# Optimization experiments

Hardware: AMD Instinct MI355X
Metric: run time of the kernel (lower is better)

Reference implementation:

```python
import jax, jax.numpy as jnp
import numpy as np

T, B, I, H = 512, 64, 1024, 1024
G = 4 * H + 1  # 4 LSTM gates + 1 boundary gate (HM-LSTM)
STDV = 1.0 / np.sqrt(H)


def setup_inputs() -> dict:
    key = jax.random.key(0)
    ks = jax.random.split(key, 5)
    u = lambda k, shape: jax.random.uniform(k, shape, jnp.float32, -STDV, STDV)
    return {
        "x": jax.random.normal(ks[0], (T, B, I), jnp.float32),
        "W_ih": u(ks[1], (G, I)),
        "W_hh": u(ks[2], (G, H)),
        "b_ih": u(ks[3], (G,)),
        "b_hh": u(ks[4], (G,)),
    }


def reference(x, W_ih, W_hh, b_ih, b_hh):
    h_dim = W_hh.shape[1]
    # Precompute input contribution for all timesteps in one big GEMM: [T,B,G]
    gx_all = jnp.einsum("tbi,gi->tbg", x, W_ih) + b_ih + b_hh
    Bsz = x.shape[1]
    h0 = jnp.zeros((Bsz, h_dim), x.dtype)
    c0 = jnp.zeros((Bsz, h_dim), x.dtype)

    def step(carry, gx):
        h, c = carry
        g = gx + h @ W_hh.T  # [B, 4H+1]
        i = jax.nn.sigmoid(g[:, :h_dim])
        f = jax.nn.sigmoid(g[:, h_dim:2 * h_dim])
        gg = jnp.tanh(g[:, 2 * h_dim:3 * h_dim])
        o = jax.nn.sigmoid(g[:, 3 * h_dim:4 * h_dim])
        z = jax.nn.sigmoid(g[:, 4 * h_dim:])  # [B,1] boundary gate
        ig = i * gg
        # HM-LSTM soft boundary: FLUSH (c=i*g) when z->1, UPDATE otherwise
        c_new = z * ig + (1.0 - z) * (f * c + ig)
        h_new = o * jnp.tanh(c_new)
        return (h_new, c_new), h_new

    (hT, cT), out = jax.lax.scan(step, (h0, c0), gx_all)
    return out, hT, cT
```

## Files before the change

### kernel.cpp

```cpp
#include <hip/hip_runtime.h>
#include <cstdint>
#include <cstddef>

typedef unsigned short u16;
typedef short bf16x8 __attribute__((ext_vector_type(8)));
typedef u16   u16x8  __attribute__((ext_vector_type(8)));
typedef float f32x4  __attribute__((ext_vector_type(4)));

#define NT  512
#define NB  64
#define NH  1024
#define NTB 32768
#define G4  4096

#define AS1C(p) ((const __attribute__((address_space(1))) void*)(p))
#define AS3(p)  ((__attribute__((address_space(3))) void*)(p))

__device__ __forceinline__ float b2f(u16 u){
  return __uint_as_float(((unsigned)u) << 16);
}
__device__ __forceinline__ u16 f2b(float f){
  unsigned u = __float_as_uint(f);
  return (u16)((u + 0x7fffu + ((u >> 16) & 1u)) >> 16);
}
__device__ __forceinline__ float fsigmoid(float x){
  return __builtin_amdgcn_rcpf(1.f + __builtin_amdgcn_exp2f(-1.442695041f * x));
}
__device__ __forceinline__ float ftanh(float x){
  return 2.f * __builtin_amdgcn_rcpf(1.f + __builtin_amdgcn_exp2f(-2.885390082f * x)) - 1.f;
}

__global__ void cvt_bf16(const float* __restrict__ in, u16* __restrict__ out, int n8){
  int stride = gridDim.x * blockDim.x;
  for (int i = blockIdx.x * blockDim.x + threadIdx.x; i < n8; i += stride){
    const float4* p = (const float4*)(in + (size_t)i * 8);
    float4 a = p[0], b = p[1];
    u16x8 r;
    r[0]=f2b(a.x); r[1]=f2b(a.y); r[2]=f2b(a.z); r[3]=f2b(a.w);
    r[4]=f2b(b.x); r[5]=f2b(b.y); r[6]=f2b(b.z); r[7]=f2b(b.w);
    *(u16x8*)(out + (size_t)i * 8) = r;
  }
}

__global__ void zpre_kernel(const float* __restrict__ x, const float* __restrict__ Wih,
                            const float* __restrict__ b_ih, const float* __restrict__ b_hh,
                            float* __restrict__ zp){
  int gw   = (blockIdx.x * 256 + threadIdx.x) >> 6;
  int lane = threadIdx.x & 63;
  const float* wz = Wih + (size_t)4096 * 1024;
  float4 wv[4];
  #pragma unroll
  for (int j = 0; j < 4; ++j) wv[j] = *(const float4*)&wz[lane*16 + j*4];
  float bz = b_ih[4096] + b_hh[4096];
  for (int r = gw; r < NTB; r += 1024){
    const float* xr = x + (size_t)r * 1024 + lane * 16;
    float s = 0.f;
    #pragma unroll
    for (int j = 0; j < 4; ++j){
      float4 xv = *(const float4*)&xr[j*4];
      s += xv.x*wv[j].x + xv.y*wv[j].y + xv.z*wv[j].z + xv.w*wv[j].w;
    }
    #pragma unroll
    for (int o = 32; o > 0; o >>= 1) s += __shfl_down(s, o);
    if (lane == 0) zp[r] = s + bz;
  }
}

template<typename GT>
__global__ __launch_bounds__(256, 2) void gemm_gx(
    const u16* __restrict__ Xb, const u16* __restrict__ Wb,
    const float* __restrict__ b_ih, const float* __restrict__ b_hh,
    GT* __restrict__ gx)
{
  __shared__ u16 As[128*32];
  __shared__ u16 Bs[128*32];
  const int tid  = threadIdx.x;
  const int lane = tid & 63, wave = tid >> 6;
  const int wr = wave >> 1, wc = wave & 1;
  const int m0 = (blockIdx.x & 255) * 128;
  const int n0 = (blockIdx.x >> 8) * 128;
  const int srow = wave * 16 + (lane >> 2);
  const int scol = (lane & 3) * 8;
  const u16* gA = Xb + (size_t)(m0 + srow) * 1024 + scol;
  const u16* gB = Wb + (size_t)(n0 + srow) * 1024 + scol;
  char* lA = (char*)As + wave * 1024;
  char* lB = (char*)Bs + wave * 1024;
  const int fr = lane & 15, fo = (lane >> 4) * 8;

  f32x4 acc[4][4] = {};
  for (int k0 = 0; k0 < 1024; k0 += 32){
    __syncthreads();
    __builtin_amdgcn_global_load_lds(AS1C(gA + k0),            AS3(lA),        16, 0, 0);
    __builtin_amdgcn_global_load_lds(AS1C(gA + 64*1024 + k0),  AS3(lA + 4096), 16, 0, 0);
    __builtin_amdgcn_global_load_lds(AS1C(gB + k0),            AS3(lB),        16, 0, 0);
    __builtin_amdgcn_global_load_lds(AS1C(gB + 64*1024 + k0),  AS3(lB + 4096), 16, 0, 0);
    __syncthreads();
    bf16x8 a[4], b[4];
    #pragma unroll
    for (int mi = 0; mi < 4; ++mi)
      a[mi] = *(const bf16x8*)&As[(wr*64 + mi*16 + fr)*32 + fo];
    #pragma unroll
    for (int ni = 0; ni < 4; ++ni)
      b[ni] = *(const bf16x8*)&Bs[(wc*64 + ni*16 + fr)*32 + fo];
    #pragma unroll
    for (int mi = 0; mi < 4; ++mi)
      #pragma unroll
      for (int ni = 0; ni < 4; ++ni)
        acc[mi][ni] = __builtin_amdgcn_mfma_f32_16x16x32_bf16(a[mi], b[ni], acc[mi][ni], 0, 0, 0);
  }
  const int orow = (lane >> 4) * 4, ocol = lane & 15;
  #pragma unroll
  for (int ni = 0; ni < 4; ++ni){
    const int g = n0 + wc*64 + ni*16 + ocol;
    const float bias = b_ih[g] + b_hh[g];
    #pragma unroll
    for (int mi = 0; mi < 4; ++mi){
      const size_t rb = (size_t)(m0 + wr*64 + mi*16 + orow);
      #pragma unroll
      for (int r = 0; r < 4; ++r){
        float v = acc[mi][ni][r] + bias;
        if constexpr (sizeof(GT) == 4)
          __builtin_nontemporal_store(v, (float*)gx + (rb + r)*G4 + g);
        else
          __builtin_nontemporal_store(f2b(v), (u16*)gx + (rb + r)*G4 + g);
      }
    }
  }
}

__device__ __forceinline__ float ld_gx(const float* p){ return __builtin_nontemporal_load(p); }
__device__ __forceinline__ float ld_gx(const u16* p){ return b2f(__builtin_nontemporal_load(p)); }

template<typename GT>
__global__ __launch_bounds__(256, 1) void hmlstm_scan(
    const u16* __restrict__ Whh, const GT* __restrict__ gx,
    const float* __restrict__ zpre, u16* __restrict__ hbase,
    float* __restrict__ out, unsigned* __restrict__ bar)
{
  const int tid  = threadIdx.x;
  const int lane = tid & 63, wave = tid >> 6;
  const int wg = blockIdx.x;
  const int mb = wg >> 6, hb = wg & 63;
  const int fr = lane & 15, hi4 = lane >> 4;
  const int b_l = tid >> 4, h_l = tid & 15;
  const int browg = mb*16 + b_l;

  __shared__ u16  hs[16*1024];
  __shared__ float glds[4][16][16];
  __shared__ float zpart[4][16];
  __shared__ u16  wz[1024];

  ((unsigned long long*)wz)[tid] = ((const unsigned long long*)(Whh + (size_t)4096*1024))[tid];

  const int grow = wave*1024 + hb*16 + fr;
  bf16x8 Bw[32];
  #pragma unroll
  for (int kc = 0; kc < 32; ++kc)
    Bw[kc] = *(const bf16x8*)&Whh[(size_t)grow*1024 + kc*32 + hi4*8];
  #pragma unroll
  for (int kc = 0; kc < 32; ++kc)
    asm volatile("" : "+v"(Bw[kc]));

  {
    u16* p = hbase + (size_t)mb*16384 + hb*256 + tid;
    unsigned z = 0;
    asm volatile("global_store_short %0, %1, off sc0 sc1" :: "v"(p), "v"(z) : "memory");
    asm volatile("s_waitcnt vmcnt(0)" ::: "memory");
  }
  unsigned* myflag = bar + mb*256 + hb*4 + wave;
  const unsigned* gflags = bar + mb*256;
  if (lane == 0){
    unsigned one = 1;
    asm volatile("global_store_dword %0, %1, off sc0 sc1" :: "v"(myflag), "v"(one) : "memory");
  }

  float c_reg = 0.f;

  for (int t = 0; t < NT; ++t){
    const u16* hc = hbase + (size_t)t * 65536;
    u16*       hn = hbase + (size_t)(t + 1) * 65536;

    float gxl[4];
    const GT* gp = gx + ((size_t)t*64 + mb*16 + hi4*4)*G4 + wave*1024 + hb*16 + fr;
    #pragma unroll
    for (int r = 0; r < 4; ++r) gxl[r] = ld_gx(gp + (size_t)r*G4);
    float zpc = zpre[t*64 + browg];

    {
      const unsigned* fp = gflags + lane*4;
      unsigned tgt = (unsigned)(t + 1);
      uint4 fv;
      unsigned mn;
      do {
        asm volatile("global_load_dwordx4 %0, %1, off sc0 sc1\n\ts_waitcnt vmcnt(0)"
                     : "=v"(fv) : "v"(fp) : "memory");
        mn = min(min(fv.x, fv.y), min(fv.z, fv.w));
      } while (!__all((int)(mn >= tgt)));
      __builtin_amdgcn_sched_barrier(0);
    }

    {
      const char* gsrc = (const char*)hc + (size_t)mb * 32768;
      char* hsB = (char*)hs;
      #pragma unroll
      for (int j = 0; j < 8; ++j){
        int chunk = wave*8 + j;
        int row   = chunk >> 1;
        int srcoff = row*2048 + ((((chunk & 1)*64 + lane)*16) ^ ((row & 7) << 4));
        __builtin_amdgcn_global_load_lds(AS1C(gsrc + srcoff), AS3(hsB + chunk*1024), 16, 0, 0);
      }
    }
    asm volatile("s_waitcnt vmcnt(0)" ::: "memory");
    __builtin_amdgcn_sched_barrier(0);
    __syncthreads();

    f32x4 acc[4] = {}, az = {};
    #pragma unroll
    for (int kc = 0; kc < 32; ++kc){
      bf16x8 a = *(const bf16x8*)((char*)hs + fr*2048 + ((kc*64 + hi4*16) ^ ((fr&7)<<4)));
      acc[kc & 3] = __builtin_amdgcn_mfma_f32_16x16x32_bf16(a, Bw[kc], acc[kc & 3], 0, 0, 0);
    }
    #pragma unroll
    for (int q = 0; q < 8; ++q){
      int kcz = wave*8 + q;
      bf16x8 a  = *(const bf16x8*)((char*)hs + fr*2048 + ((kcz*64 + hi4*16) ^ ((fr&7)<<4)));
      bf16x8 bz = *(const bf16x8*)&wz[kcz*32 + hi4*8];
      az = __builtin_amdgcn_mfma_f32_16x16x32_bf16(a, bz, az, 0, 0, 0);
    }
    f32x4 ac = (acc[0] + acc[1]) + (acc[2] + acc[3]);

    #pragma unroll
    for (int r = 0; r < 4; ++r){
      float v = ac[r] + gxl[r];
      float s = (wave == 2) ? ftanh(v) : fsigmoid(v);
      glds[wave][hi4*4 + r][fr] = s;
    }
    if (fr == 0){
      #pragma unroll
      for (int r = 0; r < 4; ++r) zpart[wave][hi4*4 + r] = az[r];
    }
    __syncthreads();

    float iv = glds[0][b_l][h_l], fvg = glds[1][b_l][h_l];
    float gv = glds[2][b_l][h_l], ov = glds[3][b_l][h_l];
    float zs = zpart[0][b_l] + zpart[1][b_l] + zpart[2][b_l] + zpart[3][b_l];
    float zv = fsigmoid(zpc + zs);
    float ig = iv * gv;
    float cn = zv*ig + (1.f - zv)*(fvg*c_reg + ig);
    float hv_ = ov * ftanh(cn);
    c_reg = cn;
    const int hoff = browg*1024 + hb*16 + h_l;

    {
      unsigned hv16 = (unsigned)f2b(hv_);
      asm volatile("global_store_short %0, %1, off sc0 sc1" :: "v"(hn + hoff), "v"(hv16) : "memory");
      asm volatile("s_waitcnt vmcnt(0)" ::: "memory");
      if (lane == 0){
        unsigned pv = (unsigned)(t + 2);
        asm volatile("global_store_dword %0, %1, off sc0 sc1" :: "v"(myflag), "v"(pv) : "memory");
      }
    }

    __builtin_nontemporal_store(hv_, out + (size_t)t*65536 + hoff);
    if (t == NT-1){
      out[(size_t)NT*65536 + hoff] = hv_;
      out[(size_t)NT*65536 + 65536 + hoff] = cn;
    }
  }
}

extern "C" void kernel_launch(void* const* d_in, const int* in_sizes, int n_in,
                              void* d_out, int out_size, void* d_ws, size_t ws_size,
                              hipStream_t stream)
{
  (void)in_sizes; (void)n_in; (void)out_size;
  const float* x    = (const float*)d_in[0];
  const float* Wih  = (const float*)d_in[1];
  const float* Whh  = (const float*)d_in[2];
  const float* b_ih = (const float*)d_in[3];
  const float* b_hh = (const float*)d_in[4];
  float* out = (float*)d_out;

  size_t off = 0;
  auto alloc = [&](size_t bytes)->void*{
    void* p = (char*)d_ws + off;
    off = (off + bytes + 255) & ~(size_t)255;
    return p;
  };
  u16*  xb    = (u16*) alloc((size_t)NTB*1024*2);
  u16*  wihb  = (u16*) alloc((size_t)4097*1024*2);
  u16*  whhb  = (u16*) alloc((size_t)4097*1024*2);
  u16*  hbase = (u16*) alloc((size_t)(NT+1)*65536*2);
  float* zp   = (float*)alloc((size_t)NTB*4);
  unsigned* bar = (unsigned*)alloc(4096);
  bool g32 = (ws_size >= off + (size_t)NTB*G4*4);
  void* gxp = (char*)d_ws + off;

  hipMemsetAsync(bar, 0, 4096, stream);
  cvt_bf16<<<dim3(2048), dim3(256), 0, stream>>>(x,   xb,   NTB*1024/8);
  cvt_bf16<<<dim3(512),  dim3(256), 0, stream>>>(Wih, wihb, 4097*1024/8);
  cvt_bf16<<<dim3(512),  dim3(256), 0, stream>>>(Whh, whhb, 4097*1024/8);
  zpre_kernel<<<dim3(256), dim3(256), 0, stream>>>(x, Wih, b_ih, b_hh, zp);
  if (g32){
    gemm_gx<float><<<dim3(8192), dim3(256), 0, stream>>>(xb, wihb, b_ih, b_hh, (float*)gxp);
    hmlstm_scan<float><<<dim3(256), dim3(256), 0, stream>>>(whhb, (const float*)gxp, zp,
                                                            hbase, out, bar);
  } else {
    gemm_gx<u16><<<dim3(8192), dim3(256), 0, stream>>>(xb, wihb, b_ih, b_hh, (u16*)gxp);
    hmlstm_scan<u16><<<dim3(256), dim3(256), 0, stream>>>(whhb, (const u16*)gxp, zp,
                                                          hbase, out, bar);
  }
}
```

Before: 3.902 ms.

## Pack timestep tag with bf16 hidden state to replace flag barrier

Each hidden value is now stored as a 32-bit word holding the bf16 value and a 16-bit timestep tag. Consumers poll the data itself and re-read only the rows whose tags are stale, so the separate flag array, the store-wait-flag sequence and the flag spin loop are gone. The per-step hidden history becomes a double buffer, and the gx/zpre loads are issued as async asm loads so they overlap the polling. This doubles the bytes read per step for h and moves the LDS fill from a direct global-to-LDS copy to register unpacking, and it relies on the 16-bit tag staying unambiguous and on 64-bit ordering within the double buffer.

```diff
diff --git a/kernel.cpp b/kernel.cpp
--- a/kernel.cpp
+++ b/kernel.cpp
@@ -128,14 +128,11 @@
   }
 }
 
-__device__ __forceinline__ float ld_gx(const float* p){ return __builtin_nontemporal_load(p); }
-__device__ __forceinline__ float ld_gx(const u16* p){ return b2f(__builtin_nontemporal_load(p)); }
-
 template<typename GT>
 __global__ __launch_bounds__(256, 1) void hmlstm_scan(
     const u16* __restrict__ Whh, const GT* __restrict__ gx,
-    const float* __restrict__ zpre, u16* __restrict__ hbase,
-    float* __restrict__ out, unsigned* __restrict__ bar)
+    const float* __restrict__ zpre, unsigned* __restrict__ hdw,
+    float* __restrict__ out)
 {
   const int tid  = threadIdx.x;
   const int lane = tid & 63, wave = tid >> 6;
@@ -162,56 +159,76 @@
     asm volatile("" : "+v"(Bw[kc]));
 
   {
-    u16* p = hbase + (size_t)mb*16384 + hb*256 + tid;
-    unsigned z = 0;
-    asm volatile("global_store_short %0, %1, off sc0 sc1" :: "v"(p), "v"(z) : "memory");
-    asm volatile("s_waitcnt vmcnt(0)" ::: "memory");
-  }
-  unsigned* myflag = bar + mb*256 + hb*4 + wave;
-  const unsigned* gflags = bar + mb*256;
-  if (lane == 0){
-    unsigned one = 1;
-    asm volatile("global_store_dword %0, %1, off sc0 sc1" :: "v"(myflag), "v"(one) : "memory");
+    unsigned* p = hdw + (size_t)browg*1024 + hb*16 + h_l;
+    unsigned v0 = 1u;
+    asm volatile("global_store_dword %0, %1, off sc0 sc1" :: "v"(p), "v"(v0) : "memory");
   }
 
   float c_reg = 0.f;
 
   for (int t = 0; t < NT; ++t){
-    const u16* hc = hbase + (size_t)t * 65536;
-    u16*       hn = hbase + (size_t)(t + 1) * 65536;
-
-    float gxl[4];
-    const GT* gp = gx + ((size_t)t*64 + mb*16 + hi4*4)*G4 + wave*1024 + hb*16 + fr;
-    #pragma unroll
-    for (int r = 0; r < 4; ++r) gxl[r] = ld_gx(gp + (size_t)r*G4);
-    float zpc = zpre[t*64 + browg];
-
+    const unsigned* src = hdw + (size_t)(t & 1) * 65536;
+    unsigned*       dst = hdw + (size_t)((t + 1) & 1) * 65536;
+    const unsigned tgt = (unsigned)(t + 1);
+
+    uint4 v[16];
+    #pragma unroll
+    for (int j = 0; j < 16; ++j){
+      const uint4* p = (const uint4*)(src + (size_t)(mb*16 + j)*1024 + tid*4);
+      asm volatile("global_load_dwordx4 %0, %1, off sc0 sc1" : "=v"(v[j]) : "v"(p) : "memory");
+    }
+    float gxl[4]; float zpc;
     {
-      const unsigned* fp = gflags + lane*4;
-      unsigned tgt = (unsigned)(t + 1);
-      uint4 fv;
-      unsigned mn;
-      do {
-        asm volatile("global_load_dwordx4 %0, %1, off sc0 sc1\n\ts_waitcnt vmcnt(0)"
-                     : "=v"(fv) : "v"(fp) : "memory");
-        mn = min(min(fv.x, fv.y), min(fv.z, fv.w));
-      } while (!__all((int)(mn >= tgt)));
+      const GT* gp = gx + ((size_t)t*64 + mb*16 + hi4*4)*G4 + wave*1024 + hb*16 + fr;
+      if constexpr (sizeof(GT) == 4){
+        #pragma unroll
+        for (int r = 0; r < 4; ++r)
+          asm volatile("global_load_dword %0, %1, off nt" : "=v"(gxl[r]) : "v"((const float*)gp + (size_t)r*G4) : "memory");
+      } else {
+        #pragma unroll
+        for (int r = 0; r < 4; ++r)
+          asm volatile("global_load_ushort %0, %1, off nt" : "=v"(*(unsigned*)&gxl[r]) : "v"((const u16*)gp + (size_t)r*G4) : "memory");
+      }
+      asm volatile("global_load_dword %0, %1, off" : "=v"(zpc) : "v"(zpre + t*64 + browg) : "memory");
+    }
+    asm volatile("s_waitcnt vmcnt(5)" ::: "memory");
+    __builtin_amdgcn_sched_barrier(0);
+
+    unsigned pend = 0;
+    #pragma unroll
+    for (int j = 0; j < 16; ++j){
+      bool ok = ((v[j].x & 0xFFFFu) == tgt) & ((v[j].y & 0xFFFFu) == tgt)
+              & ((v[j].z & 0xFFFFu) == tgt) & ((v[j].w & 0xFFFFu) == tgt);
+      pend |= ok ? 0u : (1u << j);
+    }
+    while (__any((int)(pend != 0u))){
+      #pragma unroll
+      for (int j = 0; j < 16; ++j){
+        if (__any((int)((pend >> j) & 1u))){
+          const uint4* p = (const uint4*)(src + (size_t)(mb*16 + j)*1024 + tid*4);
+          asm volatile("global_load_dwordx4 %0, %1, off sc0 sc1" : "=v"(v[j]) : "v"(p) : "memory");
+        }
+      }
+      asm volatile("s_waitcnt vmcnt(0)" ::: "memory");
       __builtin_amdgcn_sched_barrier(0);
-    }
-
-    {
-      const char* gsrc = (const char*)hc + (size_t)mb * 32768;
-      char* hsB = (char*)hs;
-      #pragma unroll
-      for (int j = 0; j < 8; ++j){
-        int chunk = wave*8 + j;
-        int row   = chunk >> 1;
-        int srcoff = row*2048 + ((((chunk & 1)*64 + lane)*16) ^ ((row & 7) << 4));
-        __builtin_amdgcn_global_load_lds(AS1C(gsrc + srcoff), AS3(hsB + chunk*1024), 16, 0, 0);
+      #pragma unroll
+      for (int j = 0; j < 16; ++j){
+        if ((pend >> j) & 1u){
+          bool ok = ((v[j].x & 0xFFFFu) == tgt) & ((v[j].y & 0xFFFFu) == tgt)
+                  & ((v[j].z & 0xFFFFu) == tgt) & ((v[j].w & 0xFFFFu) == tgt);
+          if (ok) pend &= ~(1u << j);
+        }
       }
     }
-    asm volatile("s_waitcnt vmcnt(0)" ::: "memory");
-    __builtin_amdgcn_sched_barrier(0);
+
+    #pragma unroll
+    for (int j = 0; j < 16; ++j){
+      unsigned p0 = (v[j].x >> 16) | (v[j].y & 0xFFFF0000u);
+      unsigned p1 = (v[j].z >> 16) | (v[j].w & 0xFFFF0000u);
+      uint2 pw = {p0, p1};
+      int addr = j*2048 + ((((tid>>1)*16) ^ ((j&7)<<4)) + (tid&1)*8);
+      *(uint2*)((char*)hs + addr) = pw;
+    }
     __syncthreads();
 
     f32x4 acc[4] = {}, az = {};
@@ -229,10 +246,19 @@
     }
     f32x4 ac = (acc[0] + acc[1]) + (acc[2] + acc[3]);
 
+    asm volatile("s_waitcnt vmcnt(0)" ::: "memory");
+    __builtin_amdgcn_sched_barrier(0);
+
+    if constexpr (sizeof(GT) != 4){
+      #pragma unroll
+      for (int r = 0; r < 4; ++r)
+        gxl[r] = __uint_as_float((*(unsigned*)&gxl[r]) << 16);
+    }
+
     #pragma unroll
     for (int r = 0; r < 4; ++r){
-      float v = ac[r] + gxl[r];
-      float s = (wave == 2) ? ftanh(v) : fsigmoid(v);
+      float vv = ac[r] + gxl[r];
+      float s = (wave == 2) ? ftanh(vv) : fsigmoid(vv);
       glds[wave][hi4*4 + r][fr] = s;
     }
     if (fr == 0){
@@ -252,13 +278,8 @@
     const int hoff = browg*1024 + hb*16 + h_l;
 
     {
-      unsigned hv16 = (unsigned)f2b(hv_);
-      asm volatile("global_store_short %0, %1, off sc0 sc1" :: "v"(hn + hoff), "v"(hv16) : "memory");
-      asm volatile("s_waitcnt vmcnt(0)" ::: "memory");
-      if (lane == 0){
-        unsigned pv = (unsigned)(t + 2);
-        asm volatile("global_store_dword %0, %1, off sc0 sc1" :: "v"(myflag), "v"(pv) : "memory");
-      }
+      unsigned pv = ((unsigned)f2b(hv_) << 16) | (unsigned)(t + 2);
+      asm volatile("global_store_dword %0, %1, off sc0 sc1" :: "v"(dst + hoff), "v"(pv) : "memory");
     }
 
     __builtin_nontemporal_store(hv_, out + (size_t)t*65536 + hoff);
@@ -290,24 +311,21 @@
   u16*  xb    = (u16*) alloc((size_t)NTB*1024*2);
   u16*  wihb  = (u16*) alloc((size_t)4097*1024*2);
   u16*  whhb  = (u16*) alloc((size_t)4097*1024*2);
-  u16*  hbase = (u16*) alloc((size_t)(NT+1)*65536*2);
+  unsigned* hdw = (unsigned*)alloc((size_t)2*65536*4);
   float* zp   = (float*)alloc((size_t)NTB*4);
-  unsigned* bar = (unsigned*)alloc(4096);
   bool g32 = (ws_size >= off + (size_t)NTB*G4*4);
   void* gxp = (char*)d_ws + off;
 
-  hipMemsetAsync(bar, 0, 4096, stream);
+  hipMemsetAsync(hdw, 0, (size_t)2*65536*4, stream);
   cvt_bf16<<<dim3(2048), dim3(256), 0, stream>>>(x,   xb,   NTB*1024/8);
   cvt_bf16<<<dim3(512),  dim3(256), 0, stream>>>(Wih, wihb, 4097*1024/8);
   cvt_bf16<<<dim3(512),  dim3(256), 0, stream>>>(Whh, whhb, 4097*1024/8);
   zpre_kernel<<<dim3(256), dim3(256), 0, stream>>>(x, Wih, b_ih, b_hh, zp);
   if (g32){
     gemm_gx<float><<<dim3(8192), dim3(256), 0, stream>>>(xb, wihb, b_ih, b_hh, (float*)gxp);
-    hmlstm_scan<float><<<dim3(256), dim3(256), 0, stream>>>(whhb, (const float*)gxp, zp,
-                                                            hbase, out, bar);
+    hmlstm_scan<float><<<dim3(256), dim3(256), 0, stream>>>(whhb, (const float*)gxp, zp, hdw, out);
   } else {
     gemm_gx<u16><<<dim3(8192), dim3(256), 0, stream>>>(xb, wihb, b_ih, b_hh, (u16*)gxp);
-    hmlstm_scan<u16><<<dim3(256), dim3(256), 0, stream>>>(whhb, (const u16*)gxp, zp,
-                                                          hbase, out, bar);
-  }
-}
+    hmlstm_scan<u16><<<dim3(256), dim3(256), 0, stream>>>(whhb, (const u16*)gxp, zp, hdw, out);
+  }
+}
```

Result: faster. 3.520 ms (-9.8%).
